# Kernel optimization log

Hardware: AMD Instinct MI355X
Metric: run time of the kernel (lower is better)

Reference implementation:

```python
import jax, jax.numpy as jnp
import numpy as np

N, E, G = 50000, 400000, 512
F_IN, H = 128, 128  # OPS_LENGTH, hidden_channels
NEG_SLOPE = 0.2
BN_EPS = 1e-5


def seg_softmax(e, idx, n):
    m = jax.ops.segment_max(e, idx, num_segments=n)
    ex = jnp.exp(e - m[idx])
    s = jax.ops.segment_sum(ex, idx, num_segments=n)
    return ex / (s[idx] + 1e-16)


def gatv2(x, src, dst, Wl, Wr, att, b, n):
    # PyG GATv2Conv, heads=1: e = att . leaky_relu(Wl x_src + Wr x_dst),
    # alpha = softmax over incoming edges per dst, out = sum alpha * Wl x_src + b
    xl = x @ Wl
    xr = x @ Wr
    z = jax.nn.leaky_relu(xl[src] + xr[dst], NEG_SLOPE)  # [E, out]
    e = jnp.einsum('ed,d->e', z, att)
    a = seg_softmax(e, dst, n)
    return jax.ops.segment_sum(xl[src] * a[:, None], dst, num_segments=n) + b


def bn_eval(x, g, b, m, v):
    return (x - m) * jax.lax.rsqrt(v + BN_EPS) * g + b


def setup_inputs() -> dict:
    key = jax.random.key(0)
    ks = jax.random.split(key, 40)
    d = {}
    d['x'] = jax.random.normal(ks[0], (N, F_IN), dtype=jnp.float32)
    d['edge_index'] = jax.random.randint(ks[1], (2, E), 0, N)
    d['batch'] = jnp.sort(jax.random.randint(ks[2], (N,), 0, G))
    def lin(k, i, o, s=None):
        s = s if s is not None else 1.0 / np.sqrt(i)
        return jax.random.normal(k, (i, o), dtype=jnp.float32) * s
    # conv1: 128->128, conv2: 128->256, conv3: 256->128
    d['Wl1'] = lin(ks[3], F_IN, H); d['Wr1'] = lin(ks[4], F_IN, H)
    d['att1'] = jax.random.normal(ks[5], (H,), dtype=jnp.float32) * 0.1
    d['b1'] = jnp.zeros((H,), jnp.float32)
    d['Wl2'] = lin(ks[6], H, 2 * H); d['Wr2'] = lin(ks[7], H, 2 * H)
    d['att2'] = jax.random.normal(ks[8], (2 * H,), dtype=jnp.float32) * 0.1
    d['b2'] = jnp.zeros((2 * H,), jnp.float32)
    d['Wl3'] = lin(ks[9], 2 * H, H); d['Wr3'] = lin(ks[10], 2 * H, H)
    d['att3'] = jax.random.normal(ks[11], (H,), dtype=jnp.float32) * 0.1
    d['b3'] = jnp.zeros((H,), jnp.float32)
    d['Wlin1'] = lin(ks[12], H, 128); d['blin1'] = jnp.zeros((128,), jnp.float32)
    d['Wlin2'] = lin(ks[13], 128, 64); d['blin2'] = jnp.zeros((64,), jnp.float32)
    d['Wlin3'] = lin(ks[14], 64, 2); d['blin3'] = jnp.zeros((2,), jnp.float32)
    for name, dim, i in [('bng', H, 15), ('bn1', 128, 19), ('bn2', 64, 23)]:
        d[name + '_g'] = jax.random.uniform(ks[i], (dim,), minval=0.5, maxval=1.5)
        d[name + '_b'] = jax.random.normal(ks[i + 1], (dim,), dtype=jnp.float32) * 0.1
        d[name + '_m'] = jax.random.normal(ks[i + 2], (dim,), dtype=jnp.float32) * 0.1
        d[name + '_v'] = jax.random.uniform(ks[i + 3], (dim,), minval=0.5, maxval=1.5)
    return d


def reference(x, edge_index, batch, Wl1, Wr1, att1, b1, Wl2, Wr2, att2, b2,
              Wl3, Wr3, att3, b3, Wlin1, blin1, Wlin2, blin2, Wlin3, blin3,
              bng_g, bng_b, bng_m, bng_v, bn1_g, bn1_b, bn1_m, bn1_v,
              bn2_g, bn2_b, bn2_m, bn2_v):
    src, dst = edge_index[0], edge_index[1]
    h = jax.nn.relu(gatv2(x, src, dst, Wl1, Wr1, att1, b1, N))
    h = jax.nn.relu(gatv2(h, src, dst, Wl2, Wr2, att2, b2, N))
    h = gatv2(h, src, dst, Wl3, Wr3, att3, b3, N)
    # global_mean_pool
    sums = jax.ops.segment_sum(h, batch, num_segments=G)
    cnt = jax.ops.segment_sum(jnp.ones((N,), h.dtype), batch, num_segments=G)
    g = sums / jnp.maximum(cnt, 1.0)[:, None]
    # dropout p=0.5 is identity in eval mode; BatchNorms in eval mode
    g = bn_eval(g, bng_g, bng_b, bng_m, bng_v)
    g = bn_eval(jax.nn.relu(g @ Wlin1 + blin1), bn1_g, bn1_b, bn1_m, bn1_v)
    g = bn_eval(jax.nn.relu(g @ Wlin2 + blin2), bn2_g, bn2_b, bn2_m, bn2_v)
    return jax.nn.relu(g @ Wlin3 + blin3)
```

## Files before the change

### kernel.cpp

```cpp
#include <hip/hip_runtime.h>
#include <math.h>

#define N_NODES 50000
#define NPAD 50048
#define N_EDGES 400000
#define N_GRAPHS 512
#define NEG_SLOPE 0.2f
#define BN_EPS 1e-5f
#define SCAN_BLOCKS 49

#define C6 0.8656170245333781f
#define C4 0.5770780163555854f
#define THR_LOG2 11.541560327111708f

typedef __attribute__((ext_vector_type(8))) short bf16x8;
typedef __attribute__((ext_vector_type(4))) float f32x4;

__device__ __forceinline__ ushort f2b(float f) {
    unsigned u = __float_as_uint(f);
    unsigned r = (u + 0x7fffu + ((u >> 16) & 1u)) >> 16;
    return (ushort)r;
}
__device__ __forceinline__ float b2f(ushort u) {
    return __uint_as_float((unsigned)u << 16);
}
__device__ __forceinline__ float b2f_lo(unsigned u) { return __uint_as_float(u << 16); }
__device__ __forceinline__ float b2f_hi(unsigned u) { return __uint_as_float(u & 0xffff0000u); }

__device__ __forceinline__ void gld_lds16(const void* g, void* l) {
    __builtin_amdgcn_global_load_lds(
        (const __attribute__((address_space(1))) void*)g,
        (__attribute__((address_space(3))) void*)l, 16, 0, 0);
}

__global__ void cvt_kernel(const float* __restrict__ in, ushort* __restrict__ out,
                           int total4) {
    const int i = blockIdx.x * 256 + threadIdx.x;
    if (i >= total4) return;
    float4 v = *(const float4*)(in + (size_t)i * 4);
    ushort4 o;
    o.x = f2b(v.x); o.y = f2b(v.y); o.z = f2b(v.z); o.w = f2b(v.w);
    *(ushort4*)(out + (size_t)i * 4) = o;
}

__global__ void wcvt_all_kernel(const float* __restrict__ Wl1, const float* __restrict__ Wr1,
                                const float* __restrict__ Wl2, const float* __restrict__ Wr2,
                                const float* __restrict__ Wl3, const float* __restrict__ Wr3,
                                ushort* __restrict__ wt1, ushort* __restrict__ wt2,
                                ushort* __restrict__ wt3) {
    const int i = blockIdx.x * 256 + threadIdx.x;
    if (i < 32768) {
        const int m = i >> 7, k = i & 127;
        const float v = (m < 128) ? Wl1[k * 128 + m] : Wr1[k * 128 + (m - 128)];
        wt1[i] = f2b(v);
    } else if (i < 98304) {
        const int j = i - 32768;
        const int m = j >> 7, k = j & 127;
        const float v = (m < 256) ? Wl2[k * 256 + m] : Wr2[k * 256 + (m - 256)];
        wt2[j] = f2b(v);
    } else if (i < 163840) {
        const int j = i - 98304;
        const int m = j >> 8, k = j & 255;
        const float v = (m < 128) ? Wl3[k * 128 + m] : Wr3[k * 128 + (m - 128)];
        wt3[j] = f2b(v);
    }
}

__global__ __launch_bounds__(256) void gemm_bf16_kernel(
    const ushort* __restrict__ A, const ushort* __restrict__ Bt,
    ushort* __restrict__ C, int K, int M) {
    __shared__ ushort As[4096];
    __shared__ ushort Bs[4096];
    const int tid = threadIdx.x;
    const int row0 = blockIdx.x * 128;
    const int col0 = blockIdx.y * 128;
    const int w = tid >> 6, lane = tid & 63;
    const int wr = (w >> 1) * 64, wc = (w & 1) * 64;
    const int lr = lane & 15, kg = lane >> 4;

    char* as_b = (char*)As;
    char* bs_b = (char*)Bs;

    const int o0 = tid * 16;
    const int o1 = o0 + 4096;
    const int u0 = o0 ^ ((o0 >> 3) & 0x30);
    const int u1 = o1 ^ ((o1 >> 3) & 0x30);
    const int ar0 = u0 >> 6, ac0 = (u0 >> 4) & 3;
    const int ar1 = (u1 >> 6) & 127, ac1 = (u1 >> 4) & 3;

    const ushort* ga0 = A + (size_t)(row0 + ar0) * K + ac0 * 8;
    const ushort* ga1 = A + (size_t)(row0 + ar1) * K + ac1 * 8;
    const ushort* gb0 = Bt + (size_t)(col0 + ar0) * K + ac0 * 8;
    const ushort* gb1 = Bt + (size_t)(col0 + ar1) * K + ac1 * 8;

    char* da0 = as_b + w * 1024;
    char* da1 = as_b + 4096 + w * 1024;
    char* db0 = bs_b + w * 1024;
    char* db1 = bs_b + 4096 + w * 1024;

    const int sxor = ((lr >> 1) & 3) << 4;
    const int abase = (((wr + lr) * 64) + kg * 16) ^ sxor;
    const int bbase = (((wc + lr) * 64) + kg * 16) ^ sxor;

    f32x4 acc[4][4];
#pragma unroll
    for (int i = 0; i < 4; ++i)
#pragma unroll
        for (int j = 0; j < 4; ++j) acc[i][j] = (f32x4){0.f, 0.f, 0.f, 0.f};

    for (int k0 = 0; k0 < K; k0 += 32) {
        gld_lds16(ga0, da0);
        gld_lds16(ga1, da1);
        gld_lds16(gb0, db0);
        gld_lds16(gb1, db1);
        ga0 += 32; ga1 += 32; gb0 += 32; gb1 += 32;
        __syncthreads();
        bf16x8 af[4], bfr[4];
#pragma unroll
        for (int mi = 0; mi < 4; ++mi)
            af[mi] = *(const bf16x8*)(as_b + abase + mi * 1024);
#pragma unroll
        for (int ni = 0; ni < 4; ++ni)
            bfr[ni] = *(const bf16x8*)(bs_b + bbase + ni * 1024);
#pragma unroll
        for (int mi = 0; mi < 4; ++mi)
#pragma unroll
            for (int ni = 0; ni < 4; ++ni)
                acc[mi][ni] = __builtin_amdgcn_mfma_f32_16x16x32_bf16(
                    af[mi], bfr[ni], acc[mi][ni], 0, 0, 0);
        __syncthreads();
    }
#pragma unroll
    for (int mi = 0; mi < 4; ++mi)
#pragma unroll
        for (int ni = 0; ni < 4; ++ni)
#pragma unroll
            for (int j = 0; j < 4; ++j) {
                const int r = row0 + wr + mi * 16 + kg * 4 + j;
                C[(size_t)r * M + col0 + wc + ni * 16 + lr] = f2b(acc[mi][ni][j]);
            }
}

__global__ void deg_count_kernel(const int* __restrict__ ei, int* __restrict__ deg) {
    const int e = blockIdx.x * 256 + threadIdx.x;
    if (e < N_EDGES) atomicAdd(&deg[ei[N_EDGES + e]], 1);
}

__global__ __launch_bounds__(256) void scanA_kernel(const int* __restrict__ deg,
                                                    int* __restrict__ rowp,
                                                    int* __restrict__ bsum) {
    const int t = threadIdx.x, b = blockIdx.x;
    const int i0 = b * 1024 + t * 4;
    int4 d = make_int4(0, 0, 0, 0);
    if (i0 + 3 < N_NODES) d = *(const int4*)(deg + i0);
    else {
        if (i0 + 0 < N_NODES) d.x = deg[i0 + 0];
        if (i0 + 1 < N_NODES) d.y = deg[i0 + 1];
        if (i0 + 2 < N_NODES) d.z = deg[i0 + 2];
    }
    const int tsum = d.x + d.y + d.z + d.w;
    int inc = tsum;
    const int lane = t & 63, wave = t >> 6;
#pragma unroll
    for (int o = 1; o < 64; o <<= 1) {
        int v = __shfl_up(inc, o, 64);
        if (lane >= o) inc += v;
    }
    __shared__ int wsum[4];
    if (lane == 63) wsum[wave] = inc;
    __syncthreads();
    int wbase = 0;
#pragma unroll
    for (int ww = 0; ww < 4; ++ww)
        if (ww < wave) wbase += wsum[ww];
    const int texcl = wbase + inc - tsum;
    int4 o4;
    o4.x = texcl;
    o4.y = o4.x + d.x;
    o4.z = o4.y + d.y;
    o4.w = o4.z + d.z;
    if (i0 + 3 < N_NODES) *(int4*)(rowp + i0) = o4;
    else {
        if (i0 + 0 < N_NODES) rowp[i0 + 0] = o4.x;
        if (i0 + 1 < N_NODES) rowp[i0 + 1] = o4.y;
        if (i0 + 2 < N_NODES) rowp[i0 + 2] = o4.z;
    }
    if (t == 255) bsum[b] = wbase + inc;
}

__global__ __launch_bounds__(256) void scanC_kernel(const int* __restrict__ bsum,
                                                    int* __restrict__ rowp) {
    const int t = threadIdx.x, b = blockIdx.x;
    __shared__ int base_s;
    if (t < 64) {
        int v = (t < b) ? bsum[t] : 0;
#pragma unroll
        for (int o = 32; o; o >>= 1) v += __shfl_xor(v, o, 64);
        if (t == 0) base_s = v;
    }
    __syncthreads();
    const int base = base_s;
    const int i0 = b * 1024 + t * 4;
    if (base != 0) {
        if (i0 + 3 < N_NODES) {
            int4 v = *(int4*)(rowp + i0);
            v.x += base; v.y += base; v.z += base; v.w += base;
            *(int4*)(rowp + i0) = v;
        } else {
            if (i0 + 0 < N_NODES) rowp[i0 + 0] += base;
            if (i0 + 1 < N_NODES) rowp[i0 + 1] += base;
            if (i0 + 2 < N_NODES) rowp[i0 + 2] += base;
        }
    }
    if (b == 0 && t == 0) rowp[N_NODES] = N_EDGES;
}

__global__ void csr_fill_kernel(const int* __restrict__ ei, const int* __restrict__ rowp,
                                int* __restrict__ cursor, int* __restrict__ csr_src) {
    const int e = blockIdx.x * 256 + threadIdx.x;
    if (e >= N_EDGES) return;
    const int d = ei[N_EDGES + e];
    const int pos = atomicAdd(&cursor[d], 1);
    csr_src[rowp[d] + pos] = ei[e];
}

template <int VEC>
__device__ __forceinline__ void sm_upd(float& m, float& s, float* acc, float p,
                                       const float* l) {
    if (p > m + THR_LOG2) {
        const float sc = __builtin_amdgcn_exp2f(m - p);
        s = s * sc + 1.f;
#pragma unroll
        for (int k = 0; k < VEC; ++k) acc[k] = acc[k] * sc + l[k];
        m = p;
    } else {
        const float w = __builtin_amdgcn_exp2f(p - m);
        s += w;
#pragma unroll
        for (int k = 0; k < VEC; ++k) acc[k] += w * l[k];
    }
}

template <int FO, int VEC>
__device__ __forceinline__ float edge_dot(const ushort* __restrict__ hx, int src, int co,
                                          const float* a6, const float* a4,
                                          const float* r, float* l) {
    if constexpr (VEC == 8) {
        uint4 t = *(const uint4*)(hx + (size_t)src * (2 * FO) + co);
        l[0] = b2f_lo(t.x); l[1] = b2f_hi(t.x);
        l[2] = b2f_lo(t.y); l[3] = b2f_hi(t.y);
        l[4] = b2f_lo(t.z); l[5] = b2f_hi(t.z);
        l[6] = b2f_lo(t.w); l[7] = b2f_hi(t.w);
    } else {
        uint2 t = *(const uint2*)(hx + (size_t)src * (2 * FO) + co);
        l[0] = b2f_lo(t.x); l[1] = b2f_hi(t.x);
        l[2] = b2f_lo(t.y); l[3] = b2f_hi(t.y);
    }
    float p = 0.f;
#pragma unroll
    for (int k = 0; k < VEC; ++k) {
        const float z = l[k] + r[k];
        p = fmaf(a6[k], z, p);
        p = fmaf(a4[k], fabsf(z), p);
    }
    return p;
}

template <int FO, int VEC>
__global__ __launch_bounds__(256) void gat_edge_kernel(
    const int* __restrict__ rowp, const int* __restrict__ csr_src,
    const ushort* __restrict__ hx,
    const float* __restrict__ att, const float* __restrict__ bias,
    float* __restrict__ outf, ushort* __restrict__ outb, int do_relu) {
    const int d = blockIdx.x * 8 + (threadIdx.x >> 5);
    const int lane = threadIdx.x & 31;
    if (d >= N_NODES) return;
    const int co = lane * VEC;

    float a6[VEC], a4[VEC], r[VEC];
#pragma unroll
    for (int k = 0; k < VEC; ++k) {
        const float av = att[co + k];
        a6[k] = C6 * av;
        a4[k] = C4 * av;
        r[k] = b2f(hx[(size_t)d * (2 * FO) + FO + co + k]);
    }

    const int jb = rowp[d], je = rowp[d + 1];
    float m0 = -INFINITY, s0 = 0.f, m1 = -INFINITY, s1 = 0.f;
    float acc0[VEC] = {}, acc1[VEC] = {};

    int j = jb;
    for (; j + 1 < je; j += 2) {
        const int sA = csr_src[j + 0];
        const int sB = csr_src[j + 1];
        float lA[VEC], lB[VEC];
        float pA = edge_dot<FO, VEC>(hx, sA, co, a6, a4, r, lA);
        float pB = edge_dot<FO, VEC>(hx, sB, co, a6, a4, r, lB);
#pragma unroll
        for (int o = 16; o; o >>= 1) {
            pA += __shfl_xor(pA, o, 64);
            pB += __shfl_xor(pB, o, 64);
        }
        sm_upd<VEC>(m0, s0, acc0, pA, lA);
        sm_upd<VEC>(m1, s1, acc1, pB, lB);
    }
    if (j < je) {
        const int sA = csr_src[j];
        float lA[VEC];
        float pA = edge_dot<FO, VEC>(hx, sA, co, a6, a4, r, lA);
#pragma unroll
        for (int o = 16; o; o >>= 1) pA += __shfl_xor(pA, o, 64);
        sm_upd<VEC>(m0, s0, acc0, pA, lA);
    }

    float s, acc[VEC];
    if (je > jb) {
        const float M = fmaxf(m0, m1);
        const float sc0 = __builtin_amdgcn_exp2f(m0 - M);
        const float sc1 = __builtin_amdgcn_exp2f(m1 - M);
        s = s0 * sc0 + s1 * sc1;
#pragma unroll
        for (int k = 0; k < VEC; ++k) acc[k] = acc0[k] * sc0 + acc1[k] * sc1;
    } else {
        s = 0.f;
#pragma unroll
        for (int k = 0; k < VEC; ++k) acc[k] = 0.f;
    }

    const float inv = 1.f / (s + 1e-16f);
#pragma unroll
    for (int k = 0; k < VEC; ++k) {
        float v = acc[k] * inv + bias[co + k];
        if (do_relu) v = fmaxf(v, 0.f);
        acc[k] = v;
    }
    if (outf) {
#pragma unroll
        for (int k = 0; k < VEC; k += 4)
            *(float4*)(outf + (size_t)d * FO + co + k) =
                make_float4(acc[k], acc[k + 1], acc[k + 2], acc[k + 3]);
    }
    if (outb) {
#pragma unroll
        for (int k = 0; k < VEC; k += 4) {
            ushort4 o;
            o.x = f2b(acc[k]); o.y = f2b(acc[k + 1]);
            o.z = f2b(acc[k + 2]); o.w = f2b(acc[k + 3]);
            *(ushort4*)(outb + (size_t)d * FO + co + k) = o;
        }
    }
}

__global__ void gstart_kernel(const int* __restrict__ batch, int* __restrict__ gstart) {
    const int i = blockIdx.x * 256 + threadIdx.x;
    if (i >= N_NODES) return;
    const int b = batch[i];
    if (i == 0) {
        for (int g = 0; g <= b; ++g) gstart[g] = 0;
    } else {
        const int pb = batch[i - 1];
        for (int g = pb + 1; g <= b; ++g) gstart[g] = i;
    }
    if (i == N_NODES - 1) {
        for (int g = b + 1; g <= N_GRAPHS; ++g) gstart[g] = N_NODES;
    }
}

__global__ __launch_bounds__(128) void pool2_kernel(const float* __restrict__ h,
                                                    const int* __restrict__ gstart,
                                                    float* __restrict__ gsum,
                                                    float* __restrict__ gcnt) {
    const int g = blockIdx.x, t = threadIdx.x;
    const int b = gstart[g], e = gstart[g + 1];
    float s = 0.f;
    for (int i = b; i < e; ++i) s += h[(size_t)i * 128 + t];
    gsum[g * 128 + t] = s;
    if (t == 0) gcnt[g] = (float)(e - b);
}

__global__ __launch_bounds__(128) void mlp_kernel(
    const float* __restrict__ gsum, const float* __restrict__ gcnt,
    const float* __restrict__ W1, const float* __restrict__ b1,
    const float* __restrict__ W2, const float* __restrict__ b2,
    const float* __restrict__ W3, const float* __restrict__ b3,
    const float* __restrict__ bng_g, const float* __restrict__ bng_b,
    const float* __restrict__ bng_m, const float* __restrict__ bng_v,
    const float* __restrict__ bn1_g, const float* __restrict__ bn1_b,
    const float* __restrict__ bn1_m, const float* __restrict__ bn1_v,
    const float* __restrict__ bn2_g, const float* __restrict__ bn2_b,
    const float* __restrict__ bn2_m, const float* __restrict__ bn2_v,
    float* __restrict__ out) {
    __shared__ float s0[128], s1[128], s2[64];
    const int g = blockIdx.x, t = threadIdx.x;
    const float cnt = fmaxf(gcnt[g], 1.f);
    float v = gsum[g * 128 + t] / cnt;
    v = (v - bng_m[t]) * rsqrtf(bng_v[t] + BN_EPS) * bng_g[t] + bng_b[t];
    s0[t] = v;
    __syncthreads();
    float a1 = b1[t];
    for (int i = 0; i < 128; ++i) a1 += s0[i] * W1[i * 128 + t];
    a1 = fmaxf(a1, 0.f);
    a1 = (a1 - bn1_m[t]) * rsqrtf(bn1_v[t] + BN_EPS) * bn1_g[t] + bn1_b[t];
    s1[t] = a1;
    __syncthreads();
    if (t < 64) {
        float a2 = b2[t];
        for (int i = 0; i < 128; ++i) a2 += s1[i] * W2[i * 64 + t];
        a2 = fmaxf(a2, 0.f);
        a2 = (a2 - bn2_m[t]) * rsqrtf(bn2_v[t] + BN_EPS) * bn2_g[t] + bn2_b[t];
        s2[t] = a2;
    }
    __syncthreads();
    if (t < 2) {
        float a3 = b3[t];
        for (int i = 0; i < 64; ++i) a3 += s2[i] * W3[i * 2 + t];
        out[g * 2 + t] = fmaxf(a3, 0.f);
    }
}

extern "C" void kernel_launch(void* const* d_in, const int* in_sizes, int n_in,
                              void* d_out, int out_size, void* d_ws, size_t ws_size,
                              hipStream_t stream) {
    const float* x = (const float*)d_in[0];
    const int* ei = (const int*)d_in[1];
    const int* batch = (const int*)d_in[2];
    const float* Wl1 = (const float*)d_in[3];
    const float* Wr1 = (const float*)d_in[4];
    const float* att1 = (const float*)d_in[5];
    const float* b1 = (const float*)d_in[6];
    const float* Wl2 = (const float*)d_in[7];
    const float* Wr2 = (const float*)d_in[8];
    const float* att2 = (const float*)d_in[9];
    const float* b2 = (const float*)d_in[10];
    const float* Wl3 = (const float*)d_in[11];
    const float* Wr3 = (const float*)d_in[12];
    const float* att3 = (const float*)d_in[13];
    const float* b3 = (const float*)d_in[14];
    const float* Wlin1 = (const float*)d_in[15];
    const float* blin1 = (const float*)d_in[16];
    const float* Wlin2 = (const float*)d_in[17];
    const float* blin2 = (const float*)d_in[18];
    const float* Wlin3 = (const float*)d_in[19];
    const float* blin3 = (const float*)d_in[20];
    const float* bng_g = (const float*)d_in[21];
    const float* bng_b = (const float*)d_in[22];
    const float* bng_m = (const float*)d_in[23];
    const float* bng_v = (const float*)d_in[24];
    const float* bn1_g = (const float*)d_in[25];
    const float* bn1_b = (const float*)d_in[26];
    const float* bn1_m = (const float*)d_in[27];
    const float* bn1_v = (const float*)d_in[28];
    const float* bn2_g = (const float*)d_in[29];
    const float* bn2_b = (const float*)d_in[30];
    const float* bn2_m = (const float*)d_in[31];
    const float* bn2_v = (const float*)d_in[32];

    float* ws = (float*)d_ws;
    ushort* hx = (ushort*)ws;
    float* h3 = (float*)(hx + (size_t)NPAD * 512);
    ushort* hbf = (ushort*)(h3 + (size_t)N_NODES * 128);
    ushort* wt1 = hbf + (size_t)NPAD * 256;
    ushort* wt2 = wt1 + 256 * 128;
    ushort* wt3 = wt2 + 512 * 128;
    int* deg = (int*)(wt3 + 256 * 256);
    int* cursor = deg + N_NODES;
    int* rowp = cursor + N_NODES;
    int* csr_src = rowp + N_NODES + 1;
    int* gstart = csr_src + N_EDGES;
    int* bsum = gstart + N_GRAPHS + 1;
    float* gsum = (float*)(bsum + SCAN_BLOCKS);
    float* gcnt = gsum + (size_t)N_GRAPHS * 128;

    const int eb = (N_EDGES + 255) / 256;

    hipMemsetAsync(deg, 0, (size_t)N_NODES * 2 * 4, stream);
    deg_count_kernel<<<eb, 256, 0, stream>>>(ei, deg);
    scanA_kernel<<<SCAN_BLOCKS, 256, 0, stream>>>(deg, rowp, bsum);
    scanC_kernel<<<SCAN_BLOCKS, 256, 0, stream>>>(bsum, rowp);
    csr_fill_kernel<<<eb, 256, 0, stream>>>(ei, rowp, cursor, csr_src);
    gstart_kernel<<<(N_NODES + 255) / 256, 256, 0, stream>>>(batch, gstart);

    wcvt_all_kernel<<<640, 256, 0, stream>>>(Wl1, Wr1, Wl2, Wr2, Wl3, Wr3, wt1, wt2, wt3);
    cvt_kernel<<<(N_NODES * 128 / 4 + 255) / 256, 256, 0, stream>>>(
        x, hbf, N_NODES * 128 / 4);

    const int nb = (N_NODES + 7) / 8;
    const int gx = NPAD / 128;

    gemm_bf16_kernel<<<dim3(gx, 2), 256, 0, stream>>>(hbf, wt1, hx, 128, 256);
    gat_edge_kernel<128, 4><<<nb, 256, 0, stream>>>(rowp, csr_src, hx,
                                                    att1, b1, nullptr, hbf, 1);
    gemm_bf16_kernel<<<dim3(gx, 4), 256, 0, stream>>>(hbf, wt2, hx, 128, 512);
    gat_edge_kernel<256, 8><<<nb, 256, 0, stream>>>(rowp, csr_src, hx,
                                                    att2, b2, nullptr, hbf, 1);
    gemm_bf16_kernel<<<dim3(gx, 2), 256, 0, stream>>>(hbf, wt3, hx, 256, 256);
    gat_edge_kernel<128, 4><<<nb, 256, 0, stream>>>(rowp, csr_src, hx,
                                                    att3, b3, h3, nullptr, 0);

    pool2_kernel<<<N_GRAPHS, 128, 0, stream>>>(h3, gstart, gsum, gcnt);

    mlp_kernel<<<N_GRAPHS, 128, 0, stream>>>(
        gsum, gcnt, Wlin1, blin1, Wlin2, blin2, Wlin3, blin3,
        bng_g, bng_b, bng_m, bng_v, bn1_g, bn1_b, bn1_m, bn1_v,
        bn2_g, bn2_b, bn2_m, bn2_v, (float*)d_out);
}
```

Measured before the change: 273.6 us.

## Schedule GAT destination nodes in degree-sorted order via counting sort

Adds a degree histogram, a descending scan and a permutation kernel that sort destination nodes by in-degree, and the three GAT edge kernels now process nodes in that order. Each block of eight warps then holds nodes of similar degree, which is meant to reduce imbalance and tail effects where heavy nodes finish last. The cost is three extra small launches, a memset, and scattered output writes and self-row reads, since neighbouring warps no longer handle neighbouring nodes.

```diff
diff --git a/kernel.cpp b/kernel.cpp
--- a/kernel.cpp
+++ b/kernel.cpp
@@ -8,6 +8,7 @@
 #define NEG_SLOPE 0.2f
 #define BN_EPS 1e-5f
 #define SCAN_BLOCKS 49
+#define NBIN 256
 
 #define C6 0.8656170245333781f
 #define C4 0.5770780163555854f
@@ -224,6 +225,31 @@
     csr_src[rowp[d] + pos] = ei[e];
 }
 
+__global__ void dhist_kernel(const int* __restrict__ deg, int* __restrict__ hist) {
+    const int i = blockIdx.x * 256 + threadIdx.x;
+    if (i < N_NODES) atomicAdd(&hist[min(deg[i], NBIN - 1)], 1);
+}
+
+__global__ __launch_bounds__(NBIN) void dscan_kernel(const int* __restrict__ hist,
+                                                     int* __restrict__ base) {
+    __shared__ int h[NBIN];
+    const int t = threadIdx.x;
+    h[t] = hist[t];
+    __syncthreads();
+    int s = 0;
+    for (int b = t + 1; b < NBIN; ++b) s += h[b];
+    base[t] = s;
+}
+
+__global__ void dperm_kernel(const int* __restrict__ deg, const int* __restrict__ base,
+                             int* __restrict__ bcur, int* __restrict__ perm) {
+    const int i = blockIdx.x * 256 + threadIdx.x;
+    if (i >= N_NODES) return;
+    const int b = min(deg[i], NBIN - 1);
+    const int pos = atomicAdd(&bcur[b], 1);
+    perm[base[b] + pos] = i;
+}
+
 template <int VEC>
 __device__ __forceinline__ void sm_upd(float& m, float& s, float* acc, float p,
                                        const float* l) {
@@ -269,12 +295,13 @@
 template <int FO, int VEC>
 __global__ __launch_bounds__(256) void gat_edge_kernel(
     const int* __restrict__ rowp, const int* __restrict__ csr_src,
-    const ushort* __restrict__ hx,
+    const int* __restrict__ perm, const ushort* __restrict__ hx,
     const float* __restrict__ att, const float* __restrict__ bias,
     float* __restrict__ outf, ushort* __restrict__ outb, int do_relu) {
-    const int d = blockIdx.x * 8 + (threadIdx.x >> 5);
+    const int di = blockIdx.x * 8 + (threadIdx.x >> 5);
     const int lane = threadIdx.x & 31;
-    if (d >= N_NODES) return;
+    if (di >= N_NODES) return;
+    const int d = perm[di];
     const int co = lane * VEC;
 
     float a6[VEC], a4[VEC], r[VEC];
@@ -469,17 +496,26 @@
     int* csr_src = rowp + N_NODES + 1;
     int* gstart = csr_src + N_EDGES;
     int* bsum = gstart + N_GRAPHS + 1;
-    float* gsum = (float*)(bsum + SCAN_BLOCKS);
+    int* hist = bsum + SCAN_BLOCKS;
+    int* hbase = hist + NBIN;
+    int* bcur = hbase + NBIN;
+    int* perm = bcur + NBIN;
+    float* gsum = (float*)(perm + N_NODES);
     float* gcnt = gsum + (size_t)N_GRAPHS * 128;
 
     const int eb = (N_EDGES + 255) / 256;
+    const int nb256 = (N_NODES + 255) / 256;
 
     hipMemsetAsync(deg, 0, (size_t)N_NODES * 2 * 4, stream);
+    hipMemsetAsync(hist, 0, (size_t)NBIN * 3 * 4, stream);
     deg_count_kernel<<<eb, 256, 0, stream>>>(ei, deg);
     scanA_kernel<<<SCAN_BLOCKS, 256, 0, stream>>>(deg, rowp, bsum);
     scanC_kernel<<<SCAN_BLOCKS, 256, 0, stream>>>(bsum, rowp);
     csr_fill_kernel<<<eb, 256, 0, stream>>>(ei, rowp, cursor, csr_src);
-    gstart_kernel<<<(N_NODES + 255) / 256, 256, 0, stream>>>(batch, gstart);
+    dhist_kernel<<<nb256, 256, 0, stream>>>(deg, hist);
+    dscan_kernel<<<1, NBIN, 0, stream>>>(hist, hbase);
+    dperm_kernel<<<nb256, 256, 0, stream>>>(deg, hbase, bcur, perm);
+    gstart_kernel<<<nb256, 256, 0, stream>>>(batch, gstart);
 
     wcvt_all_kernel<<<640, 256, 0, stream>>>(Wl1, Wr1, Wl2, Wr2, Wl3, Wr3, wt1, wt2, wt3);
     cvt_kernel<<<(N_NODES * 128 / 4 + 255) / 256, 256, 0, stream>>>(
@@ -489,13 +525,13 @@
     const int gx = NPAD / 128;
 
     gemm_bf16_kernel<<<dim3(gx, 2), 256, 0, stream>>>(hbf, wt1, hx, 128, 256);
-    gat_edge_kernel<128, 4><<<nb, 256, 0, stream>>>(rowp, csr_src, hx,
+    gat_edge_kernel<128, 4><<<nb, 256, 0, stream>>>(rowp, csr_src, perm, hx,
                                                     att1, b1, nullptr, hbf, 1);
     gemm_bf16_kernel<<<dim3(gx, 4), 256, 0, stream>>>(hbf, wt2, hx, 128, 512);
-    gat_edge_kernel<256, 8><<<nb, 256, 0, stream>>>(rowp, csr_src, hx,
+    gat_edge_kernel<256, 8><<<nb, 256, 0, stream>>>(rowp, csr_src, perm, hx,
                                                     att2, b2, nullptr, hbf, 1);
     gemm_bf16_kernel<<<dim3(gx, 2), 256, 0, stream>>>(hbf, wt3, hx, 256, 256);
-    gat_edge_kernel<128, 4><<<nb, 256, 0, stream>>>(rowp, csr_src, hx,
+    gat_edge_kernel<128, 4><<<nb, 256, 0, stream>>>(rowp, csr_src, perm, hx,
                                                     att3, b3, h3, nullptr, 0);
 
     pool2_kernel<<<N_GRAPHS, 128, 0, stream>>>(h3, gstart, gsum, gcnt);
```

Result: slower. 612.6 us (+123.9%).
